# Performance work log

Hardware: AMD Instinct MI355X
Metric: run time of the kernel (lower is better)

Reference implementation:

```python
import jax, jax.numpy as jnp
import numpy as np

N = 25000      # n_nodes
K = 16         # k_sparse (out-degree per node)
E = N * K      # n_edges
D = 12         # depth
U = 48         # units
FEATS = 2
EF = 1
EPS = 1e-5     # BatchNorm eps


def _lin(h, W, b):
    return h @ W.T + b


def _bn(h, g, b):
    # training-mode BatchNorm over dim 0 (biased variance, like torch)
    m = h.mean(0)
    v = jnp.mean((h - m) ** 2, axis=0)
    return (h - m) * jax.lax.rsqrt(v + EPS) * g + b


def setup_inputs():
    key = jax.random.key(0)
    ks = iter(jax.random.split(key, 64))

    def nrm(shape, fan):
        return jax.random.normal(next(ks), shape, dtype=jnp.float32) * float(1.0 / np.sqrt(fan))

    inp = {}
    inp['x'] = jax.random.uniform(next(ks), (N, FEATS), dtype=jnp.float32)
    inp['edge_attr'] = jax.random.uniform(next(ks), (E, EF), dtype=jnp.float32)
    src = jnp.repeat(jnp.arange(N, dtype=jnp.int32), K)            # each node has K out-edges
    dst = jax.random.randint(next(ks), (E,), 0, N, dtype=jnp.int32)
    inp['edge_index'] = jnp.stack([src, dst])                       # [2, E]
    inp['v_lin0_W'] = nrm((U, FEATS), FEATS); inp['v_lin0_b'] = nrm((U,), FEATS)
    for nm in ['vW1', 'vW2', 'vW3', 'vW4']:
        inp[nm] = nrm((D, U, U), U)
    for nm in ['vb1', 'vb2', 'vb3', 'vb4']:
        inp[nm] = nrm((D, U), U)
    inp['vbn_g'] = jnp.ones((D, U), jnp.float32); inp['vbn_b'] = jnp.zeros((D, U), jnp.float32)
    inp['e_lin0_W'] = nrm((U, EF), EF); inp['e_lin0_b'] = nrm((U,), EF)
    inp['eW'] = nrm((D, U, U), U); inp['eb'] = nrm((D, U), U)
    inp['ebn_g'] = jnp.ones((D, U), jnp.float32); inp['ebn_b'] = jnp.zeros((D, U), jnp.float32)
    inp['pW0'] = nrm((U, U), U); inp['pb0'] = nrm((U,), U)
    inp['pW1'] = nrm((U, U), U); inp['pb1'] = nrm((U,), U)
    inp['pW2'] = nrm((1, U), U); inp['pb2'] = nrm((1,), U)
    inp['zW0'] = nrm((U, U), U); inp['zb0'] = nrm((U,), U)
    inp['zW1'] = nrm((1, U), U); inp['zb1'] = nrm((1,), U)
    inp['k_sparse'] = K
    return inp


def _forward(edge_index, k_sparse, x, edge_attr, v_lin0_W, v_lin0_b, vW1, vb1, vW2, vb2, vW3, vb3, vW4, vb4, vbn_g, vbn_b, e_lin0_W, e_lin0_b, eW, eb, ebn_g, ebn_b, pW0, pb0, pW1, pb1, pW2, pb2, zW0, zb0, zW1, zb1):
    n = x.shape[0]
    src, dst = edge_index[0], edge_index[1]
    deg = jnp.maximum(jax.ops.segment_sum(jnp.ones((src.shape[0],), x.dtype), src, num_segments=n), 1.0)
    h = jax.nn.silu(_lin(x, v_lin0_W, v_lin0_b))          # [N, U]
    w = jax.nn.silu(_lin(edge_attr, e_lin0_W, e_lin0_b))  # [E, U]

    def layer(carry, p):
        h, w = carry
        W1, b1, W2, b2, W3, b3, W4, b4, gv, bv, We, be, ge, bee = p
        h1 = _lin(h, W1, b1); h2 = _lin(h, W2, b2)
        h3 = _lin(h, W3, b3); h4 = _lin(h, W4, b4)
        msg = jax.nn.sigmoid(w) * h2[dst]                                 # [E, U] gather + gate
        agg = jax.ops.segment_sum(msg, src, num_segments=n) / deg[:, None]  # scatter-mean to source node
        h_new = h + jax.nn.silu(_bn(h1 + agg, gv, bv))
        w_new = w + jax.nn.silu(_bn(_lin(w, We, be) + h3[src] + h4[dst], ge, bee))
        return (h_new, w_new), None

    (_, w), _ = jax.lax.scan(layer, (h, w), (vW1, vb1, vW2, vb2, vW3, vb3, vW4, vb4, vbn_g, vbn_b, eW, eb, ebn_g, ebn_b))

    # ParNet heuristic head: MLP then group-softmax over k_sparse edges per node
    p = jax.nn.silu(_lin(w, pW0, pb0))
    p = jax.nn.silu(_lin(p, pW1, pb1))
    p = _lin(p, pW2, pb2).reshape(-1, k_sparse)
    heu = jax.nn.softmax(p, axis=1).reshape(-1)                            # [E]
    # Z_net logZ head (mean over edges)
    logZ = jnp.mean(jax.nn.relu(_lin(w, zW0, zb0)) @ zW1.T + zb1, axis=0)  # [1]
    return heu, logZ


def reference(x, edge_attr, edge_index, v_lin0_W, v_lin0_b, vW1, vb1, vW2, vb2, vW3, vb3, vW4, vb4, vbn_g, vbn_b, e_lin0_W, e_lin0_b, eW, eb, ebn_g, ebn_b, pW0, pb0, pW1, pb1, pW2, pb2, zW0, zb0, zW1, zb1, k_sparse):
    return _forward(edge_index, k_sparse, x, edge_attr, v_lin0_W, v_lin0_b, vW1, vb1, vW2, vb2, vW3, vb3, vW4, vb4, vbn_g, vbn_b, e_lin0_W, e_lin0_b, eW, eb, ebn_g, ebn_b, pW0, pb0, pW1, pb1, pW2, pb2, zW0, zb0, zW1, zb1)
```

## Files before the change

kernel.cpp:

```cpp
#include <hip/hip_runtime.h>
#include <hip/hip_bf16.h>
#include <hip/hip_fp16.h>

#define NN 25000
#define KK 16
#define EE 400000
#define DD 12
#define UU 48
#define EPSBN 1e-5f
#define RP 88
#define RPA 72

using bf16 = __hip_bfloat16;
typedef short bf16x8 __attribute__((ext_vector_type(8)));
typedef short sx8 __attribute__((ext_vector_type(8)));
typedef float f32x4 __attribute__((ext_vector_type(4)));

__device__ __forceinline__ float b2f(bf16 v){ return __bfloat162float(v); }
__device__ __forceinline__ float sigm(float x){ return 1.f/(1.f+__expf(-x)); }
__device__ __forceinline__ float siluf(float x){ return x/(1.f+__expf(-x)); }
__device__ __forceinline__ short f2bs(float f){ bf16 h=__float2bfloat16(f); return *(short*)&h; }
__device__ __forceinline__ float bs2f(short s){ bf16 h; *(short*)&h = s; return __bfloat162float(h); }
__device__ __forceinline__ short f2hs(float f){ __half h=__float2half(f); return *(short*)&h; }
__device__ __forceinline__ float hs2f(short s){ __half h; *(short*)&h = s; return __half2float(h); }

__device__ __forceinline__ float ldx(const void* p, size_t i, bool isb){
  return isb ? b2f(((const bf16*)p)[i]) : ((const float*)p)[i];
}
__device__ __forceinline__ void stout(void* p, size_t i, float v, bool isb){
  if (isb) ((bf16*)p)[i] = __float2bfloat16(v);
  else     ((float*)p)[i] = v;
}
__device__ __forceinline__ bool dflag(const void* vbng){
  return *((const unsigned*)vbng) == 0x3F803F80u;
}
#define LDSFENCE() asm volatile("s_waitcnt lgkmcnt(0)" ::: "memory")

__device__ __forceinline__ void stageW(short* BT, const void* W, size_t WOFF, bool isb, int tid){
  if (isb){
    const short* src = ((const short*)W) + WOFF;
    for (int j=tid; j<288; j+=256){
      int r=j/6, k=(j%6)*8;
      *(bf16x8*)&BT[r*RP+k] = *(const bf16x8*)(src + j*8);
    }
  } else {
    for (int i=tid;i<2304;i+=256){ int r=i/48,k=i%48; BT[r*RP+k]=f2bs(ldx(W,WOFF+i,false)); }
  }
}

__global__ void k_init_nodes(const void* __restrict__ x, const void* __restrict__ W0,
                             const void* __restrict__ b0, float* __restrict__ h,
                             float* __restrict__ stats, float* __restrict__ zpart,
                             const void* __restrict__ fl){
  const bool isb = dflag(fl);
  int gid = blockIdx.x*256 + threadIdx.x;
  if (gid < DD*12288) stats[gid] = 0.f;
  if (gid < 64) zpart[gid] = 0.f;
  if (gid < NN*UU){
    int n = gid/UU, c = gid%UU;
    float acc = ldx(b0,c,isb) + ldx(W0,c*2,isb)*ldx(x,n*2,isb) + ldx(W0,c*2+1,isb)*ldx(x,n*2+1,isb);
    h[gid] = siluf(acc);
  }
}

__global__ void k_init_edges(const void* __restrict__ ea, const void* __restrict__ W0,
                             const void* __restrict__ b0, short* __restrict__ w,
                             const void* __restrict__ fl){
  const bool isb = dflag(fl);
  int gid = blockIdx.x*256 + threadIdx.x;
  if (gid < EE*UU){
    int e = gid/UU, c = gid%UU;
    float acc = ldx(b0,c,isb) + ldx(W0,c,isb)*ldx(ea,e,isb);
    w[gid] = f2hs(siluf(acc));
  }
}

__global__ __launch_bounds__(256) void k_node(
    float* __restrict__ h, float* __restrict__ h1,
    short* __restrict__ h24, short* __restrict__ h3b,
    const void* __restrict__ W1, const void* __restrict__ W2,
    const void* __restrict__ W3, const void* __restrict__ W4,
    const void* __restrict__ b1, const void* __restrict__ b2,
    const void* __restrict__ b3, const void* __restrict__ b4,
    const void* __restrict__ gv, const void* __restrict__ bv,
    const float* __restrict__ stats, int ctl, const void* __restrict__ fl)
{
  const bool isb = dflag(fl);
  const int d = ctl>>1, apply = ctl&1;
  const size_t WOFF = (size_t)d*UU*UU, BOFF = (size_t)d*UU;
  __shared__ alignas(16) short BT[4][48*RP];
  __shared__ alignas(16) short AT[4][16*RP];
  __shared__ float bL[4][UU];
  __shared__ float scV[96];
  __shared__ float sred[96];
  int tid = threadIdx.x, lane = tid&63, wid = tid>>6;
  const void* Ws[4] = {W1,W2,W3,W4};
  const void* bs[4] = {b1,b2,b3,b4};
  #pragma unroll
  for (int m=0;m<4;m++) stageW(BT[m], Ws[m], WOFF, isb, tid);
  for (int i=tid;i<4*768;i+=256){ int m=i/768, j=i%768; int r=j/16,k=48+(j%16); BT[m][r*RP+k]=0; }
  for (int i=tid;i<4*256;i+=256){ int wv=i/256, j=i%256; int r=j/16,k=48+(j%16); AT[wv][r*RP+k]=0; }
  if (tid<192) bL[tid/48][tid%48] = ldx(bs[tid/48],BOFF+(tid%48),isb);
  if (apply && tid<96){
    const float* sp = stats + (size_t)(d-1)*12288;
    float s=0.f;
    for (int k2=0;k2<64;k2++) s += sp[k2*96+tid];
    sred[tid]=s;
  }
  __syncthreads();
  if (apply && tid<48){
    float mean = sred[tid]/(float)NN;
    float var = sred[48+tid]/(float)NN - mean*mean; if (var<0.f) var=0.f;
    float sc = ldx(gv,(size_t)(d-1)*48+tid,isb) * rsqrtf(var+EPSBN);
    scV[tid]=sc; scV[48+tid]=ldx(bv,(size_t)(d-1)*48+tid,isb) - mean*sc;
  }
  __syncthreads();

  int quad = lane>>4, lrow = lane&15;
  short* A = AT[wid];
  int gw = blockIdx.x*4+wid, gws = gridDim.x*4;
  const int NT = (NN+15)/16;
  for (int t=gw; t<NT; t+=gws){
    int nb = t*16;
    #pragma unroll
    for (int j=0;j<3;j++){
      int f = lane+64*j; int r=f/12, c4=f%12; int n=nb+r;
      short4 s4; s4.x=0;s4.y=0;s4.z=0;s4.w=0;
      if (n<NN){
        size_t gi = (size_t)n*48 + c4*4;
        float4 hv = *(const float4*)&h[gi];
        if (apply){
          float4 yv = *(const float4*)&h1[gi];
          int c0=c4*4;
          hv.x += siluf(scV[c0+0]*yv.x + scV[48+c0+0]);
          hv.y += siluf(scV[c0+1]*yv.y + scV[48+c0+1]);
          hv.z += siluf(scV[c0+2]*yv.z + scV[48+c0+2]);
          hv.w += siluf(scV[c0+3]*yv.w + scV[48+c0+3]);
          *(float4*)&h[gi] = hv;
        }
        s4.x=f2bs(hv.x); s4.y=f2bs(hv.y); s4.z=f2bs(hv.z); s4.w=f2bs(hv.w);
      }
      *(short4*)&A[r*RP + c4*4] = s4;
    }
    LDSFENCE();
    bf16x8 a0 = *(const bf16x8*)&A[lrow*RP + quad*8];
    bf16x8 a1 = *(const bf16x8*)&A[lrow*RP + 32 + quad*8];
    #pragma unroll
    for (int m=0;m<4;m++){
      f32x4 ac0={0,0,0,0}, ac1={0,0,0,0}, ac2={0,0,0,0};
      bf16x8 bfr;
      bfr = *(const bf16x8*)&BT[m][(0+lrow)*RP + quad*8];      ac0=__builtin_amdgcn_mfma_f32_16x16x32_bf16(a0,bfr,ac0,0,0,0);
      bfr = *(const bf16x8*)&BT[m][(0+lrow)*RP + 32 + quad*8]; ac0=__builtin_amdgcn_mfma_f32_16x16x32_bf16(a1,bfr,ac0,0,0,0);
      bfr = *(const bf16x8*)&BT[m][(16+lrow)*RP + quad*8];     ac1=__builtin_amdgcn_mfma_f32_16x16x32_bf16(a0,bfr,ac1,0,0,0);
      bfr = *(const bf16x8*)&BT[m][(16+lrow)*RP + 32 + quad*8];ac1=__builtin_amdgcn_mfma_f32_16x16x32_bf16(a1,bfr,ac1,0,0,0);
      bfr = *(const bf16x8*)&BT[m][(32+lrow)*RP + quad*8];     ac2=__builtin_amdgcn_mfma_f32_16x16x32_bf16(a0,bfr,ac2,0,0,0);
      bfr = *(const bf16x8*)&BT[m][(32+lrow)*RP + 32 + quad*8];ac2=__builtin_amdgcn_mfma_f32_16x16x32_bf16(a1,bfr,ac2,0,0,0);
      #pragma unroll
      for (int nt=0;nt<3;nt++){
        int c = nt*16+lrow;
        f32x4 ac = (nt==0)?ac0:((nt==1)?ac1:ac2);
        float bv2 = bL[m][c];
        #pragma unroll
        for (int r=0;r<4;r++){
          int n = nb + quad*4 + r;
          if (n<NN){
            float v = ac[r] + bv2;
            if (m==0) h1[(size_t)n*48+c] = v;
            else if (m==1) h24[(size_t)n*96+c*2]   = f2hs(v);
            else if (m==2) h3b[(size_t)n*48+c]     = f2hs(v);
            else           h24[(size_t)n*96+c*2+1] = f2hs(v);
          }
        }
      }
    }
  }
}

__global__ __launch_bounds__(256,4) void k_edge(
    short* __restrict__ w, short* __restrict__ tmp,
    float* __restrict__ h1, const short* __restrict__ h24,
    const short* __restrict__ h3b,
    const int* __restrict__ dst,
    const void* __restrict__ We, const void* __restrict__ eb,
    const void* __restrict__ ge, const void* __restrict__ be,
    float* __restrict__ stats, int ctl, const void* __restrict__ fl)
{
  const bool isb = dflag(fl);
  const int d = ctl>>1, apply = ctl&1;
  const size_t WOFF = (size_t)d*UU*UU, BOFF = (size_t)d*UU;
  __shared__ alignas(16) short BT[48*RP];
  __shared__ alignas(16) short AT[4][32*RPA];
  __shared__ float ebL[UU];
  __shared__ float scE[96];
  __shared__ float sred[96];
  __shared__ float sACC[4][192];
  int tid = threadIdx.x, lane = tid&63, wid = tid>>6;
  stageW(BT, We, WOFF, isb, tid);
  for (int i=tid;i<768;i+=256){ int r=i/16,k=48+(i%16); BT[r*RP+k]=0; }
  for (int i=tid;i<4*512;i+=256){ int wv=i/512, j=i%512; int tile=j/256, jj=j%256;
    int r=jj/16, k=48+(jj%16); AT[wv][tile*16*RPA + r*RPA + k]=0; }
  if (tid<48) ebL[tid]=ldx(eb,BOFF+tid,isb);
  for (int i=tid;i<768;i+=256) ((float*)sACC)[i]=0.f;
  if (apply && tid<96){
    const float* sp = stats + (size_t)(d-1)*12288 + 6144;
    float s=0.f;
    for (int k2=0;k2<64;k2++) s += sp[k2*96+tid];
    sred[tid]=s;
  }
  __syncthreads();
  if (apply && tid<48){
    float mean = sred[tid]/(float)EE;
    float var = sred[48+tid]/(float)EE - mean*mean; if (var<0.f) var=0.f;
    float sc = ldx(ge,(size_t)(d-1)*48+tid,isb) * rsqrtf(var+EPSBN);
    scE[tid]=sc; scE[48+tid]=ldx(be,(size_t)(d-1)*48+tid,isb) - mean*sc;
  }
  __syncthreads();

  int quad = lane>>4, lrow = lane&15;
  short* A0 = AT[wid];
  short* A1 = AT[wid] + 16*RPA;
  float* myStats = stats + (size_t)d*12288;
  float accY[3]={0,0,0}, accY2[3]={0,0,0}, accT[3]={0,0,0}, accT2[3]={0,0,0};
  int gw = blockIdx.x*4+wid, gws = gridDim.x*4;
  const int NP = NN/2;
  for (int p=gw; p<NP; p+=gws){
    int n0 = p*2, n1 = n0+1;
    size_t b0 = (size_t)n0*768, b1 = (size_t)n1*768;
    int4 de0 = *(const int4*)&dst[n0*16 + quad*4];
    int4 de1 = *(const int4*)&dst[n1*16 + quad*4];

    #pragma unroll
    for (int j=0;j<3;j++){
      int idx = lane + 64*j;
      int u = idx/96, jj = idx%96;
      int r = jj/6, c0 = (jj%6)*8;
      size_t bn = u ? b1 : b0;
      short* Au = u ? A1 : A0;
      sx8 w8 = *(const sx8*)&w[bn + r*48 + c0];
      float f[8];
      #pragma unroll
      for (int q=0;q<8;q++) f[q] = hs2f(w8[q]);
      if (apply){
        sx8 t8 = *(const sx8*)&tmp[bn + r*48 + c0];
        #pragma unroll
        for (int q=0;q<8;q++) f[q] += siluf(scE[c0+q]*hs2f(t8[q]) + scE[48+c0+q]);
        sx8 ws8;
        #pragma unroll
        for (int q=0;q<8;q++) ws8[q] = f2hs(f[q]);
        *(sx8*)&w[bn + r*48 + c0] = ws8;
      }
      sx8 a8;
      #pragma unroll
      for (int q=0;q<8;q++) a8[q] = f2bs(f[q]);
      *(sx8*)&Au[r*RPA + c0] = a8;
    }
    LDSFENCE();
    bf16x8 a00 = *(const bf16x8*)&A0[lrow*RPA + quad*8];
    bf16x8 a01 = *(const bf16x8*)&A0[lrow*RPA + 32 + quad*8];
    bf16x8 a10 = *(const bf16x8*)&A1[lrow*RPA + quad*8];
    bf16x8 a11 = *(const bf16x8*)&A1[lrow*RPA + 32 + quad*8];
    f32x4 acc[2][3];
    #pragma unroll
    for (int u=0;u<2;u++)
      #pragma unroll
      for (int nt=0;nt<3;nt++) acc[u][nt] = (f32x4){0,0,0,0};
    #pragma unroll
    for (int nt=0;nt<3;nt++){
      bf16x8 bf0 = *(const bf16x8*)&BT[(nt*16+lrow)*RP + quad*8];
      bf16x8 bf1 = *(const bf16x8*)&BT[(nt*16+lrow)*RP + 32 + quad*8];
      acc[0][nt]=__builtin_amdgcn_mfma_f32_16x16x32_bf16(a00,bf0,acc[0][nt],0,0,0);
      acc[0][nt]=__builtin_amdgcn_mfma_f32_16x16x32_bf16(a01,bf1,acc[0][nt],0,0,0);
      acc[1][nt]=__builtin_amdgcn_mfma_f32_16x16x32_bf16(a10,bf0,acc[1][nt],0,0,0);
      acc[1][nt]=__builtin_amdgcn_mfma_f32_16x16x32_bf16(a11,bf1,acc[1][nt],0,0,0);
    }
    #pragma unroll
    for (int u=0;u<2;u++){
      int n = n0+u;
      size_t bn = u? b1 : b0;
      short* Au = u? A1 : A0;
      int dei[4];
      if (u==0){ dei[0]=de0.x; dei[1]=de0.y; dei[2]=de0.z; dei[3]=de0.w; }
      else     { dei[0]=de1.x; dei[1]=de1.y; dei[2]=de1.z; dei[3]=de1.w; }
      #pragma unroll
      for (int nt=0;nt<3;nt++){
        int c = nt*16+lrow;
        f32x4 ac = acc[u][nt];
        float bv = ebL[c];
        float h3v = hs2f(h3b[(size_t)n*48+c]);
        float pT=0.f, pT2=0.f, pM=0.f;
        #pragma unroll
        for (int r=0;r<4;r++){
          int e = quad*4+r;
          union { unsigned uu; short2 ss; } gpair;
          gpair.uu = *(const unsigned*)&h24[(size_t)dei[r]*96 + c*2];
          float h2v = hs2f(gpair.ss.x);
          float h4v = hs2f(gpair.ss.y);
          float t = ac[r] + bv + h3v + h4v;
          tmp[bn + e*48 + c] = f2hs(t);
          pT += t; pT2 += t*t;
          float gate = bs2f(Au[e*RPA+c]);
          pM += h2v * sigm(gate);
        }
        pT  += __shfl_xor(pT,16);  pT  += __shfl_xor(pT,32);
        pT2 += __shfl_xor(pT2,16); pT2 += __shfl_xor(pT2,32);
        pM  += __shfl_xor(pM,16);  pM  += __shfl_xor(pM,32);
        accT[nt] += pT; accT2[nt] += pT2;
        if (u==0){
          if (lane<16){
            float yv = h1[(size_t)n*48+c] + pM*(1.f/16.f);
            h1[(size_t)n*48+c] = yv;
            accY[nt] += yv; accY2[nt] += yv*yv;
          }
        } else {
          if (lane>=16 && lane<32){
            float yv = h1[(size_t)n*48+c] + pM*(1.f/16.f);
            h1[(size_t)n*48+c] = yv;
            accY[nt] += yv; accY2[nt] += yv*yv;
          }
        }
      }
    }
  }
  #pragma unroll
  for (int nt=0;nt<3;nt++){
    accY[nt]  += __shfl_xor(accY[nt],16);
    accY2[nt] += __shfl_xor(accY2[nt],16);
  }
  if (lane<16){
    #pragma unroll
    for (int nt=0;nt<3;nt++){
      int c = nt*16+lane;
      sACC[wid][c]      = accY[nt];
      sACC[wid][48+c]   = accY2[nt];
      sACC[wid][96+c]   = accT[nt];
      sACC[wid][144+c]  = accT2[nt];
    }
  }
  __syncthreads();
  if (tid<192){
    float s = sACC[0][tid]+sACC[1][tid]+sACC[2][tid]+sACC[3][tid];
    int bk = (blockIdx.x&63)*96;
    if (tid<96) atomicAdd(&myStats[bk+tid], s);
    else        atomicAdd(&myStats[6144+bk+(tid-96)], s);
  }
}

__global__ __launch_bounds__(256) void k_head1(
    const short* __restrict__ w, short* __restrict__ tmp,
    const void* __restrict__ pW0, const void* __restrict__ pb0,
    const void* __restrict__ zW0, const void* __restrict__ zb0,
    const void* __restrict__ zW1,
    const void* __restrict__ ge, const void* __restrict__ be,
    const float* __restrict__ stats, float* __restrict__ zpart,
    const void* __restrict__ fl)
{
  const bool isb = dflag(fl);
  __shared__ alignas(16) short BT0[48*RP];
  __shared__ alignas(16) short BT1[48*RP];
  __shared__ alignas(16) short AT[4][16*RP];
  __shared__ float pb0L[UU], zb0L[UU], zW1L[UU];
  __shared__ float scE[96];
  __shared__ float sred[96];
  __shared__ float zS[4];
  int tid = threadIdx.x, lane = tid&63, wid = tid>>6;
  stageW(BT0, pW0, 0, isb, tid);
  stageW(BT1, zW0, 0, isb, tid);
  for (int i=tid;i<768;i+=256){ int r=i/16,k=48+(i%16); BT0[r*RP+k]=0; BT1[r*RP+k]=0; }
  for (int i=tid;i<4*256;i+=256){ int wv=i/256, j=i%256; int r=j/16,k=48+(j%16); AT[wv][r*RP+k]=0; }
  if (tid<48){ pb0L[tid]=ldx(pb0,tid,isb); zb0L[tid]=ldx(zb0,tid,isb); zW1L[tid]=ldx(zW1,tid,isb); }
  if (tid<96){
    const float* sp = stats + (size_t)(DD-1)*12288 + 6144;
    float s=0.f;
    for (int k2=0;k2<64;k2++) s += sp[k2*96+tid];
    sred[tid]=s;
  }
  __syncthreads();
  if (tid<48){
    float mean = sred[tid]/(float)EE;
    float var = sred[48+tid]/(float)EE - mean*mean; if (var<0.f) var=0.f;
    float sc = ldx(ge,(size_t)(DD-1)*48+tid,isb) * rsqrtf(var+EPSBN);
    scE[tid]=sc; scE[48+tid]=ldx(be,(size_t)(DD-1)*48+tid,isb) - mean*sc;
  }
  __syncthreads();

  int quad = lane>>4, lrow = lane&15;
  short* A = AT[wid];
  float zacc = 0.f;
  int gw = blockIdx.x*4+wid, gws = gridDim.x*4;
  for (int n=gw; n<NN; n+=gws){
    size_t basef = (size_t)n*768;
    #pragma unroll
    for (int j=0;j<2;j++){
      int idx = lane + 64*j;
      if (idx < 96){
        int r = idx/6, c0 = (idx%6)*8;
        sx8 w8 = *(const sx8*)&w[basef + r*48 + c0];
        sx8 t8 = *(const sx8*)&tmp[basef + r*48 + c0];
        sx8 a8;
        #pragma unroll
        for (int q=0;q<8;q++){
          float f = hs2f(w8[q]) + siluf(scE[c0+q]*hs2f(t8[q]) + scE[48+c0+q]);
          a8[q] = f2bs(f);
        }
        *(sx8*)&A[r*RP + c0] = a8;
      }
    }
    LDSFENCE();
    bf16x8 a0 = *(const bf16x8*)&A[lrow*RP + quad*8];
    bf16x8 a1 = *(const bf16x8*)&A[lrow*RP + 32 + quad*8];
    f32x4 p0={0,0,0,0}, p1={0,0,0,0}, p2={0,0,0,0};
    f32x4 z0={0,0,0,0}, z1={0,0,0,0}, z2={0,0,0,0};
    bf16x8 bfr;
    bfr=*(const bf16x8*)&BT0[(0+lrow)*RP+quad*8];       p0=__builtin_amdgcn_mfma_f32_16x16x32_bf16(a0,bfr,p0,0,0,0);
    bfr=*(const bf16x8*)&BT0[(0+lrow)*RP+32+quad*8];    p0=__builtin_amdgcn_mfma_f32_16x16x32_bf16(a1,bfr,p0,0,0,0);
    bfr=*(const bf16x8*)&BT0[(16+lrow)*RP+quad*8];      p1=__builtin_amdgcn_mfma_f32_16x16x32_bf16(a0,bfr,p1,0,0,0);
    bfr=*(const bf16x8*)&BT0[(16+lrow)*RP+32+quad*8];   p1=__builtin_amdgcn_mfma_f32_16x16x32_bf16(a1,bfr,p1,0,0,0);
    bfr=*(const bf16x8*)&BT0[(32+lrow)*RP+quad*8];      p2=__builtin_amdgcn_mfma_f32_16x16x32_bf16(a0,bfr,p2,0,0,0);
    bfr=*(const bf16x8*)&BT0[(32+lrow)*RP+32+quad*8];   p2=__builtin_amdgcn_mfma_f32_16x16x32_bf16(a1,bfr,p2,0,0,0);
    bfr=*(const bf16x8*)&BT1[(0+lrow)*RP+quad*8];       z0=__builtin_amdgcn_mfma_f32_16x16x32_bf16(a0,bfr,z0,0,0,0);
    bfr=*(const bf16x8*)&BT1[(0+lrow)*RP+32+quad*8];    z0=__builtin_amdgcn_mfma_f32_16x16x32_bf16(a1,bfr,z0,0,0,0);
    bfr=*(const bf16x8*)&BT1[(16+lrow)*RP+quad*8];      z1=__builtin_amdgcn_mfma_f32_16x16x32_bf16(a0,bfr,z1,0,0,0);
    bfr=*(const bf16x8*)&BT1[(16+lrow)*RP+32+quad*8];   z1=__builtin_amdgcn_mfma_f32_16x16x32_bf16(a1,bfr,z1,0,0,0);
    bfr=*(const bf16x8*)&BT1[(32+lrow)*RP+quad*8];      z2=__builtin_amdgcn_mfma_f32_16x16x32_bf16(a0,bfr,z2,0,0,0);
    bfr=*(const bf16x8*)&BT1[(32+lrow)*RP+32+quad*8];   z2=__builtin_amdgcn_mfma_f32_16x16x32_bf16(a1,bfr,z2,0,0,0);
    #pragma unroll
    for (int nt=0;nt<3;nt++){
      int c = nt*16+lrow;
      f32x4 pp = (nt==0)?p0:((nt==1)?p1:p2);
      f32x4 zz = (nt==0)?z0:((nt==1)?z1:z2);
      float pb = pb0L[c], zb = zb0L[c], zw = zW1L[c];
      #pragma unroll
      for (int r=0;r<4;r++){
        int e = quad*4+r;
        tmp[basef + e*48 + c] = f2bs(siluf(pp[r] + pb));
        float zr = zz[r] + zb;
        zacc += zw * (zr > 0.f ? zr : 0.f);
      }
    }
  }
  zacc += __shfl_xor(zacc,1); zacc += __shfl_xor(zacc,2); zacc += __shfl_xor(zacc,4);
  zacc += __shfl_xor(zacc,8); zacc += __shfl_xor(zacc,16); zacc += __shfl_xor(zacc,32);
  if (lane==0) zS[wid]=zacc;
  __syncthreads();
  if (tid==0) atomicAdd(&zpart[blockIdx.x&63], zS[0]+zS[1]+zS[2]+zS[3]);
}

__global__ __launch_bounds__(256) void k_head2(
    const short* __restrict__ tmp,
    const void* __restrict__ pW1, const void* __restrict__ pb1,
    const void* __restrict__ pW2,
    void* __restrict__ out, const void* __restrict__ fl)
{
  const bool isb = dflag(fl);
  __shared__ alignas(16) short BT[48*RP];
  __shared__ alignas(16) short AT[4][16*RP];
  __shared__ float pb1L[UU], pW2L[UU];
  int tid = threadIdx.x, lane = tid&63, wid = tid>>6;
  stageW(BT, pW1, 0, isb, tid);
  for (int i=tid;i<768;i+=256){ int r=i/16,k=48+(i%16); BT[r*RP+k]=0; }
  for (int i=tid;i<4*256;i+=256){ int wv=i/256, j=i%256; int r=j/16,k=48+(j%16); AT[wv][r*RP+k]=0; }
  if (tid<48){ pb1L[tid]=ldx(pb1,tid,isb); pW2L[tid]=ldx(pW2,tid,isb); }
  __syncthreads();

  int quad = lane>>4, lrow = lane&15;
  short* A = AT[wid];
  int gw = blockIdx.x*4+wid, gws = gridDim.x*4;
  for (int n=gw; n<NN; n+=gws){
    size_t basef = (size_t)n*768;
    #pragma unroll
    for (int j=0;j<2;j++){
      int idx = lane + 64*j;
      if (idx < 96){
        int r = idx/6, c8 = idx%6;
        *(bf16x8*)&A[r*RP + c8*8] = *(const bf16x8*)&tmp[basef + r*48 + c8*8];
      }
    }
    LDSFENCE();
    bf16x8 a0 = *(const bf16x8*)&A[lrow*RP + quad*8];
    bf16x8 a1 = *(const bf16x8*)&A[lrow*RP + 32 + quad*8];
    f32x4 q0={0,0,0,0}, q1={0,0,0,0}, q2={0,0,0,0};
    bf16x8 bfr;
    bfr=*(const bf16x8*)&BT[(0+lrow)*RP+quad*8];       q0=__builtin_amdgcn_mfma_f32_16x16x32_bf16(a0,bfr,q0,0,0,0);
    bfr=*(const bf16x8*)&BT[(0+lrow)*RP+32+quad*8];    q0=__builtin_amdgcn_mfma_f32_16x16x32_bf16(a1,bfr,q0,0,0,0);
    bfr=*(const bf16x8*)&BT[(16+lrow)*RP+quad*8];      q1=__builtin_amdgcn_mfma_f32_16x16x32_bf16(a0,bfr,q1,0,0,0);
    bfr=*(const bf16x8*)&BT[(16+lrow)*RP+32+quad*8];   q1=__builtin_amdgcn_mfma_f32_16x16x32_bf16(a1,bfr,q1,0,0,0);
    bfr=*(const bf16x8*)&BT[(32+lrow)*RP+quad*8];      q2=__builtin_amdgcn_mfma_f32_16x16x32_bf16(a0,bfr,q2,0,0,0);
    bfr=*(const bf16x8*)&BT[(32+lrow)*RP+32+quad*8];   q2=__builtin_amdgcn_mfma_f32_16x16x32_bf16(a1,bfr,q2,0,0,0);
    float pp[4] = {0.f,0.f,0.f,0.f};
    #pragma unroll
    for (int nt=0;nt<3;nt++){
      int c = nt*16+lrow;
      f32x4 qq = (nt==0)?q0:((nt==1)?q1:q2);
      float pb = pb1L[c], pw = pW2L[c];
      #pragma unroll
      for (int r=0;r<4;r++) pp[r] += pw * siluf(qq[r] + pb);
    }
    #pragma unroll
    for (int r=0;r<4;r++){
      pp[r] += __shfl_xor(pp[r],1); pp[r] += __shfl_xor(pp[r],2);
      pp[r] += __shfl_xor(pp[r],4); pp[r] += __shfl_xor(pp[r],8);
    }
    float mx = fmaxf(fmaxf(pp[0],pp[1]), fmaxf(pp[2],pp[3]));
    mx = fmaxf(mx, __shfl_xor(mx,16)); mx = fmaxf(mx, __shfl_xor(mx,32));
    float ex[4]; float se = 0.f;
    #pragma unroll
    for (int r=0;r<4;r++){ ex[r] = __expf(pp[r]-mx); se += ex[r]; }
    se += __shfl_xor(se,16); se += __shfl_xor(se,32);
    float inv = 1.f/se;
    if (lrow==0){
      #pragma unroll
      for (int r=0;r<4;r++) stout(out, (size_t)n*16 + quad*4 + r, ex[r]*inv, isb);
    }
  }
}

__global__ void k_final(const float* __restrict__ zpart, const void* __restrict__ zb1,
                        void* __restrict__ out, const void* __restrict__ fl){
  const bool isb = dflag(fl);
  int tid=threadIdx.x;
  float s = (tid<64) ? zpart[tid] : 0.f;
  s += __shfl_xor(s,1); s += __shfl_xor(s,2); s += __shfl_xor(s,4);
  s += __shfl_xor(s,8); s += __shfl_xor(s,16); s += __shfl_xor(s,32);
  if (tid==0) stout(out, EE, s/(float)EE + ldx(zb1,0,isb), isb);
}

extern "C" void kernel_launch(void* const* d_in, const int* in_sizes, int n_in,
                              void* d_out, int out_size, void* d_ws, size_t ws_size,
                              hipStream_t stream){
  (void)in_sizes; (void)n_in; (void)out_size; (void)ws_size;
  const void* x=d_in[0]; const void* ea=d_in[1];
  const int* ei=(const int*)d_in[2];
  const void* vW0=d_in[3]; const void* vb0=d_in[4];
  const void* vW1=d_in[5]; const void* vW2=d_in[6]; const void* vW3=d_in[7]; const void* vW4=d_in[8];
  const void* vb1=d_in[9]; const void* vb2=d_in[10]; const void* vb3=d_in[11]; const void* vb4=d_in[12];
  const void* vbng=d_in[13]; const void* vbnb=d_in[14];
  const void* eW0=d_in[15]; const void* eb0=d_in[16];
  const void* eW=d_in[17]; const void* ebv=d_in[18];
  const void* ebng=d_in[19]; const void* ebnb=d_in[20];
  const void* pW0=d_in[21]; const void* pb0=d_in[22];
  const void* pW1=d_in[23]; const void* pb1=d_in[24];
  const void* pW2=d_in[25]; const void* pb2=d_in[26]; (void)pb2;
  const void* zW0=d_in[27]; const void* zb0=d_in[28];
  const void* zW1=d_in[29]; const void* zb1=d_in[30];
  const int* dst = ei + EE;
  const void* fl = vbng;

  float* h   = (float*)d_ws;
  float* h1  = h  + (size_t)NN*UU;
  short* h24 = (short*)(h1 + (size_t)NN*UU);
  short* h3b = h24 + (size_t)NN*96;
  short* w   = h3b + (size_t)NN*UU;
  short* tmp = w + (size_t)EE*UU;
  float* stats = (float*)(tmp + (size_t)EE*UU);
  float* zpart = stats + DD*12288;

  k_init_nodes<<<(NN*UU+255)/256,256,0,stream>>>(x,vW0,vb0,h,stats,zpart,fl);
  k_init_edges<<<(EE*UU+255)/256,256,0,stream>>>(ea,eW0,eb0,w,fl);
  for (int d=0; d<DD; d++){
    int ctl = (d<<1) | (d>0 ? 1 : 0);
    k_node<<<512,256,0,stream>>>(h,h1,h24,h3b,
        vW1,vW2,vW3,vW4,vb1,vb2,vb3,vb4,vbng,vbnb,stats,ctl,fl);
    k_edge<<<1280,256,0,stream>>>(w,tmp,h1,h24,h3b,dst,eW,ebv,ebng,ebnb,stats,ctl,fl);
  }
  k_head1<<<1024,256,0,stream>>>(w,tmp,pW0,pb0,zW0,zb0,zW1,ebng,ebnb,stats,zpart,fl);
  k_head2<<<1024,256,0,stream>>>(tmp,pW1,pb1,pW2,d_out,fl);
  k_final<<<1,64,0,stream>>>(zpart,zb1,d_out,fl);
}
```

Measured before the change: 1.242 ms.

## Fuse edge init into first edge layer and shrink node-kernel LDS padding

Removes the separate edge-initialization kernel and computes the initial edge embedding inside the first-layer edge kernel from edge_attr, so the depth-0 pass no longer reads w back from global memory. The node kernel's LDS row pitch drops from 88 to 72 shorts, cutting shared memory per block, and its grid grows from 512 to 768 blocks to raise occupancy. The fused path reuses the scE shared buffer to hold the init weights, and the smaller pitch may change LDS bank-conflict behaviour.

```diff
diff --git a/kernel.cpp b/kernel.cpp
--- a/kernel.cpp
+++ b/kernel.cpp
@@ -9,6 +9,7 @@
 #define UU 48
 #define EPSBN 1e-5f
 #define RP 88
+#define RPN 72
 #define RPA 72
 
 using bf16 = __hip_bfloat16;
@@ -36,15 +37,15 @@
 }
 #define LDSFENCE() asm volatile("s_waitcnt lgkmcnt(0)" ::: "memory")
 
-__device__ __forceinline__ void stageW(short* BT, const void* W, size_t WOFF, bool isb, int tid){
+__device__ __forceinline__ void stageW(short* BT, const void* W, size_t WOFF, bool isb, int tid, int rp){
   if (isb){
     const short* src = ((const short*)W) + WOFF;
     for (int j=tid; j<288; j+=256){
       int r=j/6, k=(j%6)*8;
-      *(bf16x8*)&BT[r*RP+k] = *(const bf16x8*)(src + j*8);
+      *(bf16x8*)&BT[r*rp+k] = *(const bf16x8*)(src + j*8);
     }
   } else {
-    for (int i=tid;i<2304;i+=256){ int r=i/48,k=i%48; BT[r*RP+k]=f2bs(ldx(W,WOFF+i,false)); }
+    for (int i=tid;i<2304;i+=256){ int r=i/48,k=i%48; BT[r*rp+k]=f2bs(ldx(W,WOFF+i,false)); }
   }
 }
 
@@ -60,18 +61,6 @@
     int n = gid/UU, c = gid%UU;
     float acc = ldx(b0,c,isb) + ldx(W0,c*2,isb)*ldx(x,n*2,isb) + ldx(W0,c*2+1,isb)*ldx(x,n*2+1,isb);
     h[gid] = siluf(acc);
-  }
-}
-
-__global__ void k_init_edges(const void* __restrict__ ea, const void* __restrict__ W0,
-                             const void* __restrict__ b0, short* __restrict__ w,
-                             const void* __restrict__ fl){
-  const bool isb = dflag(fl);
-  int gid = blockIdx.x*256 + threadIdx.x;
-  if (gid < EE*UU){
-    int e = gid/UU, c = gid%UU;
-    float acc = ldx(b0,c,isb) + ldx(W0,c,isb)*ldx(ea,e,isb);
-    w[gid] = f2hs(siluf(acc));
   }
 }
 
@@ -88,8 +77,8 @@
   const bool isb = dflag(fl);
   const int d = ctl>>1, apply = ctl&1;
   const size_t WOFF = (size_t)d*UU*UU, BOFF = (size_t)d*UU;
-  __shared__ alignas(16) short BT[4][48*RP];
-  __shared__ alignas(16) short AT[4][16*RP];
+  __shared__ alignas(16) short BT[4][48*RPN];
+  __shared__ alignas(16) short AT[4][16*RPN];
   __shared__ float bL[4][UU];
   __shared__ float scV[96];
   __shared__ float sred[96];
@@ -97,9 +86,9 @@
   const void* Ws[4] = {W1,W2,W3,W4};
   const void* bs[4] = {b1,b2,b3,b4};
   #pragma unroll
-  for (int m=0;m<4;m++) stageW(BT[m], Ws[m], WOFF, isb, tid);
-  for (int i=tid;i<4*768;i+=256){ int m=i/768, j=i%768; int r=j/16,k=48+(j%16); BT[m][r*RP+k]=0; }
-  for (int i=tid;i<4*256;i+=256){ int wv=i/256, j=i%256; int r=j/16,k=48+(j%16); AT[wv][r*RP+k]=0; }
+  for (int m=0;m<4;m++) stageW(BT[m], Ws[m], WOFF, isb, tid, RPN);
+  for (int i=tid;i<4*768;i+=256){ int m=i/768, j=i%768; int r=j/16,k=48+(j%16); BT[m][r*RPN+k]=0; }
+  for (int i=tid;i<4*256;i+=256){ int wv=i/256, j=i%256; int r=j/16,k=48+(j%16); AT[wv][r*RPN+k]=0; }
   if (tid<192) bL[tid/48][tid%48] = ldx(bs[tid/48],BOFF+(tid%48),isb);
   if (apply && tid<96){
     const float* sp = stats + (size_t)(d-1)*12288;
@@ -140,21 +129,21 @@
         }
         s4.x=f2bs(hv.x); s4.y=f2bs(hv.y); s4.z=f2bs(hv.z); s4.w=f2bs(hv.w);
       }
-      *(short4*)&A[r*RP + c4*4] = s4;
+      *(short4*)&A[r*RPN + c4*4] = s4;
     }
     LDSFENCE();
-    bf16x8 a0 = *(const bf16x8*)&A[lrow*RP + quad*8];
-    bf16x8 a1 = *(const bf16x8*)&A[lrow*RP + 32 + quad*8];
+    bf16x8 a0 = *(const bf16x8*)&A[lrow*RPN + quad*8];
+    bf16x8 a1 = *(const bf16x8*)&A[lrow*RPN + 32 + quad*8];
     #pragma unroll
     for (int m=0;m<4;m++){
       f32x4 ac0={0,0,0,0}, ac1={0,0,0,0}, ac2={0,0,0,0};
       bf16x8 bfr;
-      bfr = *(const bf16x8*)&BT[m][(0+lrow)*RP + quad*8];      ac0=__builtin_amdgcn_mfma_f32_16x16x32_bf16(a0,bfr,ac0,0,0,0);
-      bfr = *(const bf16x8*)&BT[m][(0+lrow)*RP + 32 + quad*8]; ac0=__builtin_amdgcn_mfma_f32_16x16x32_bf16(a1,bfr,ac0,0,0,0);
-      bfr = *(const bf16x8*)&BT[m][(16+lrow)*RP + quad*8];     ac1=__builtin_amdgcn_mfma_f32_16x16x32_bf16(a0,bfr,ac1,0,0,0);
-      bfr = *(const bf16x8*)&BT[m][(16+lrow)*RP + 32 + quad*8];ac1=__builtin_amdgcn_mfma_f32_16x16x32_bf16(a1,bfr,ac1,0,0,0);
-      bfr = *(const bf16x8*)&BT[m][(32+lrow)*RP + quad*8];     ac2=__builtin_amdgcn_mfma_f32_16x16x32_bf16(a0,bfr,ac2,0,0,0);
-      bfr = *(const bf16x8*)&BT[m][(32+lrow)*RP + 32 + quad*8];ac2=__builtin_amdgcn_mfma_f32_16x16x32_bf16(a1,bfr,ac2,0,0,0);
+      bfr = *(const bf16x8*)&BT[m][(0+lrow)*RPN + quad*8];      ac0=__builtin_amdgcn_mfma_f32_16x16x32_bf16(a0,bfr,ac0,0,0,0);
+      bfr = *(const bf16x8*)&BT[m][(0+lrow)*RPN + 32 + quad*8]; ac0=__builtin_amdgcn_mfma_f32_16x16x32_bf16(a1,bfr,ac0,0,0,0);
+      bfr = *(const bf16x8*)&BT[m][(16+lrow)*RPN + quad*8];     ac1=__builtin_amdgcn_mfma_f32_16x16x32_bf16(a0,bfr,ac1,0,0,0);
+      bfr = *(const bf16x8*)&BT[m][(16+lrow)*RPN + 32 + quad*8];ac1=__builtin_amdgcn_mfma_f32_16x16x32_bf16(a1,bfr,ac1,0,0,0);
+      bfr = *(const bf16x8*)&BT[m][(32+lrow)*RPN + quad*8];     ac2=__builtin_amdgcn_mfma_f32_16x16x32_bf16(a0,bfr,ac2,0,0,0);
+      bfr = *(const bf16x8*)&BT[m][(32+lrow)*RPN + 32 + quad*8];ac2=__builtin_amdgcn_mfma_f32_16x16x32_bf16(a1,bfr,ac2,0,0,0);
       #pragma unroll
       for (int nt=0;nt<3;nt++){
         int c = nt*16+lrow;
@@ -183,6 +172,8 @@
     const int* __restrict__ dst,
     const void* __restrict__ We, const void* __restrict__ eb,
     const void* __restrict__ ge, const void* __restrict__ be,
+    const void* __restrict__ ea, const void* __restrict__ eW0,
+    const void* __restrict__ eb0,
     float* __restrict__ stats, int ctl, const void* __restrict__ fl)
 {
   const bool isb = dflag(fl);
@@ -195,7 +186,7 @@
   __shared__ float sred[96];
   __shared__ float sACC[4][192];
   int tid = threadIdx.x, lane = tid&63, wid = tid>>6;
-  stageW(BT, We, WOFF, isb, tid);
+  stageW(BT, We, WOFF, isb, tid, RP);
   for (int i=tid;i<768;i+=256){ int r=i/16,k=48+(i%16); BT[r*RP+k]=0; }
   for (int i=tid;i<4*512;i+=256){ int wv=i/512, j=i%512; int tile=j/256, jj=j%256;
     int r=jj/16, k=48+(jj%16); AT[wv][tile*16*RPA + r*RPA + k]=0; }
@@ -206,6 +197,9 @@
     float s=0.f;
     for (int k2=0;k2<64;k2++) s += sp[k2*96+tid];
     sred[tid]=s;
+  }
+  if (!apply && tid<96){
+    scE[tid] = (tid<48) ? ldx(eW0,tid,isb) : ldx(eb0,tid-48,isb);
   }
   __syncthreads();
   if (apply && tid<48){
@@ -236,19 +230,22 @@
       int r = jj/6, c0 = (jj%6)*8;
       size_t bn = u ? b1 : b0;
       short* Au = u ? A1 : A0;
-      sx8 w8 = *(const sx8*)&w[bn + r*48 + c0];
       float f[8];
-      #pragma unroll
-      for (int q=0;q<8;q++) f[q] = hs2f(w8[q]);
       if (apply){
+        sx8 w8 = *(const sx8*)&w[bn + r*48 + c0];
         sx8 t8 = *(const sx8*)&tmp[bn + r*48 + c0];
         #pragma unroll
-        for (int q=0;q<8;q++) f[q] += siluf(scE[c0+q]*hs2f(t8[q]) + scE[48+c0+q]);
-        sx8 ws8;
+        for (int q=0;q<8;q++) f[q] = hs2f(w8[q]) + siluf(scE[c0+q]*hs2f(t8[q]) + scE[48+c0+q]);
+      } else {
+        int n = u ? n1 : n0;
+        float eav = ldx(ea, (size_t)n*16 + r, isb);
         #pragma unroll
-        for (int q=0;q<8;q++) ws8[q] = f2hs(f[q]);
-        *(sx8*)&w[bn + r*48 + c0] = ws8;
-      }
+        for (int q=0;q<8;q++) f[q] = siluf(scE[c0+q]*eav + scE[48+c0+q]);
+      }
+      sx8 ws8;
+      #pragma unroll
+      for (int q=0;q<8;q++) ws8[q] = f2hs(f[q]);
+      *(sx8*)&w[bn + r*48 + c0] = ws8;
       sx8 a8;
       #pragma unroll
       for (int q=0;q<8;q++) a8[q] = f2bs(f[q]);
@@ -363,8 +360,8 @@
   __shared__ float sred[96];
   __shared__ float zS[4];
   int tid = threadIdx.x, lane = tid&63, wid = tid>>6;
-  stageW(BT0, pW0, 0, isb, tid);
-  stageW(BT1, zW0, 0, isb, tid);
+  stageW(BT0, pW0, 0, isb, tid, RP);
+  stageW(BT1, zW0, 0, isb, tid, RP);
   for (int i=tid;i<768;i+=256){ int r=i/16,k=48+(i%16); BT0[r*RP+k]=0; BT1[r*RP+k]=0; }
   for (int i=tid;i<4*256;i+=256){ int wv=i/256, j=i%256; int r=j/16,k=48+(j%16); AT[wv][r*RP+k]=0; }
   if (tid<48){ pb0L[tid]=ldx(pb0,tid,isb); zb0L[tid]=ldx(zb0,tid,isb); zW1L[tid]=ldx(zW1,tid,isb); }
@@ -456,7 +453,7 @@
   __shared__ alignas(16) short AT[4][16*RP];
   __shared__ float pb1L[UU], pW2L[UU];
   int tid = threadIdx.x, lane = tid&63, wid = tid>>6;
-  stageW(BT, pW1, 0, isb, tid);
+  stageW(BT, pW1, 0, isb, tid, RP);
   for (int i=tid;i<768;i+=256){ int r=i/16,k=48+(i%16); BT[r*RP+k]=0; }
   for (int i=tid;i<4*256;i+=256){ int wv=i/256, j=i%256; int r=j/16,k=48+(j%16); AT[wv][r*RP+k]=0; }
   if (tid<48){ pb1L[tid]=ldx(pb1,tid,isb); pW2L[tid]=ldx(pW2,tid,isb); }
@@ -555,12 +552,12 @@
   float* zpart = stats + DD*12288;
 
   k_init_nodes<<<(NN*UU+255)/256,256,0,stream>>>(x,vW0,vb0,h,stats,zpart,fl);
-  k_init_edges<<<(EE*UU+255)/256,256,0,stream>>>(ea,eW0,eb0,w,fl);
   for (int d=0; d<DD; d++){
     int ctl = (d<<1) | (d>0 ? 1 : 0);
-    k_node<<<512,256,0,stream>>>(h,h1,h24,h3b,
+    k_node<<<768,256,0,stream>>>(h,h1,h24,h3b,
         vW1,vW2,vW3,vW4,vb1,vb2,vb3,vb4,vbng,vbnb,stats,ctl,fl);
-    k_edge<<<1280,256,0,stream>>>(w,tmp,h1,h24,h3b,dst,eW,ebv,ebng,ebnb,stats,ctl,fl);
+    k_edge<<<1280,256,0,stream>>>(w,tmp,h1,h24,h3b,dst,eW,ebv,ebng,ebnb,
+        ea,eW0,eb0,stats,ctl,fl);
   }
   k_head1<<<1024,256,0,stream>>>(w,tmp,pW0,pb0,zW0,zb0,zW1,ebng,ebnb,stats,zpart,fl);
   k_head2<<<1024,256,0,stream>>>(tmp,pW1,pb1,pW2,d_out,fl);
```

Measured after the change: 1.333 ms. 7.3% more time.
